# Optimization experiments

Hardware: AMD Instinct MI355X
Metric: run time of the kernel (lower is better)

The kernel has to match this reference:

```python
import jax, jax.numpy as jnp
import numpy as np

N, E = 20000, 320000
IN_DIM, H, C, L = 256, 128, 40, 3
EPS = 1e-5


def _ln(x, g, b):
    mu = jnp.mean(x, axis=-1, keepdims=True)
    var = jnp.mean(jnp.square(x - mu), axis=-1, keepdims=True)
    return (x - mu) * jax.lax.rsqrt(var + EPS) * g + b


def setup_inputs() -> dict:
    key = jax.random.key(0)
    ks = jax.random.split(key, 24)
    s = lambda *sh: 1.0 / np.sqrt(sh[-2] if len(sh) > 1 else sh[-1])
    inp = {
        "x": jax.random.normal(ks[0], (N, IN_DIM), jnp.float32),
        "edge_index": jax.random.randint(ks[1], (2, E), 0, N, jnp.int32),
        "proj_W": jax.random.normal(ks[2], (IN_DIM, H), jnp.float32) / np.sqrt(IN_DIM),
        "proj_b": jnp.zeros((H,), jnp.float32),
        "ln0_g": jnp.ones((H,), jnp.float32),
        "ln0_b": jnp.zeros((H,), jnp.float32),
        "sim_W1": jax.random.normal(ks[3], (L, 3 * H, H), jnp.float32) / np.sqrt(3 * H),
        "sim_b1": jnp.zeros((L, H), jnp.float32),
        "sim_W2": jax.random.normal(ks[4], (L, H, 1), jnp.float32) / np.sqrt(H),
        "sim_b2": jnp.zeros((L, 1), jnp.float32),
        "W_msg": jax.random.normal(ks[5], (L, H, H), jnp.float32) / np.sqrt(H),
        "W_upd": jax.random.normal(ks[6], (L, 2 * H, H), jnp.float32) / np.sqrt(2 * H),
        "b_upd": jnp.zeros((L, H), jnp.float32),
        "ln_g": jnp.ones((L, H), jnp.float32),
        "ln_b": jnp.zeros((L, H), jnp.float32),
        "cls_W1": jax.random.normal(ks[7], (H, H // 2), jnp.float32) / np.sqrt(H),
        "cls_b1": jnp.zeros((H // 2,), jnp.float32),
        "cls_W2": jax.random.normal(ks[8], (H // 2, C), jnp.float32) / np.sqrt(H // 2),
        "cls_b2": jnp.zeros((C,), jnp.float32),
    }
    return inp


def reference(x, edge_index, proj_W, proj_b, ln0_g, ln0_b, sim_W1, sim_b1,
              sim_W2, sim_b2, W_msg, W_upd, b_upd, ln_g, ln_b,
              cls_W1, cls_b1, cls_W2, cls_b2):
    n = x.shape[0]
    # add self loops
    loops = jnp.arange(n, dtype=edge_index.dtype)
    src = jnp.concatenate([edge_index[0], loops])
    dst = jnp.concatenate([edge_index[1], loops])

    h = jax.nn.relu(_ln(x @ proj_W + proj_b, ln0_g, ln0_b))  # (N,H); dropout=eval no-op

    for l in range(L):
        x_i = h[dst]                      # (E',H)
        x_j = h[src]                      # (E',H)
        sim_in = jnp.concatenate([x_i, x_j, jnp.abs(x_i - x_j)], axis=-1)  # (E',3H)
        hmid = jax.nn.relu(sim_in @ sim_W1[l] + sim_b1[l])
        score = jax.nn.sigmoid(hmid @ sim_W2[l] + sim_b2[l])  # (E',1)
        msg = x_j @ W_msg[l]              # (E',H)
        agg = jax.ops.segment_sum(score * msg, dst, num_segments=n)  # (N,H)
        upd = jnp.concatenate([h, agg], axis=-1) @ W_upd[l] + b_upd[l]
        upd = upd + h                     # residual (identity since in==out)
        h = jax.nn.relu(_ln(upd, ln_g[l], ln_b[l]))

    logits = jax.nn.relu(h @ cls_W1 + cls_b1) @ cls_W2 + cls_b2
    return logits
```

## Files before the change

### kernel.cpp

```cpp
#include <hip/hip_runtime.h>
#include <hip/hip_bf16.h>

#define HD 128
#define LN_EPS 1e-5f

typedef __attribute__((ext_vector_type(8))) short short8;
typedef __attribute__((ext_vector_type(4))) float f32x4;

__device__ __forceinline__ unsigned short f2bf(float f) {
    union { float f; unsigned u; } v; v.f = f;
    unsigned r = (v.u + 0x7fffu + ((v.u >> 16) & 1u)) >> 16;
    return (unsigned short)r;
}

__device__ __forceinline__ unsigned cvtpk(float lo, float hi) {
    unsigned r;
    asm("v_cvt_pk_bf16_f32 %0, %1, %2" : "=v"(r) : "v"(lo), "v"(hi));
    return r;
}
__device__ __forceinline__ unsigned cvtpk_abs(float lo, float hi) {
    unsigned r;
    asm("v_cvt_pk_bf16_f32 %0, abs(%1), abs(%2)" : "=v"(r) : "v"(lo), "v"(hi));
    return r;
}
__device__ __forceinline__ unsigned absd_bf2(unsigned a, unsigned b) {
    float alo = __uint_as_float(a << 16), ahi = __uint_as_float(a & 0xffff0000u);
    float blo = __uint_as_float(b << 16), bhi = __uint_as_float(b & 0xffff0000u);
    return cvtpk_abs(alo - blo, ahi - bhi);
}

__device__ __forceinline__ float wave_sum_all(float v) {
    #pragma unroll
    for (int o = 32; o > 0; o >>= 1) v += __shfl_xor(v, o);
    return v;
}

__global__ __launch_bounds__(256) void w1bf_kernel(
    const float* __restrict__ W1, unsigned short* __restrict__ out, int total)
{
    int idx = blockIdx.x * 256 + threadIdx.x;
    if (idx >= total) return;
    int lw  = idx / 49152;
    int rem = idx - lw * 49152;
    int j  = rem & 7;
    int c  = (rem >> 3) & 15;
    int ks = (rem >> 7) & 3;
    int ct = (rem >> 9) & 7;
    int q  = rem >> 12;
    out[idx] = f2bf(W1[(size_t)lw * 49152 + (size_t)(q * 32 + ks * 8 + j) * 128 + ct * 16 + c]);
}

__global__ __launch_bounds__(256) void copy_upd_kernel(
    const float* __restrict__ W_upd, float* __restrict__ wcomb, int total)
{
    int idx = blockIdx.x * 256 + threadIdx.x;
    if (idx >= total) return;
    int l = idx / 16384, r = idx - l * 16384;
    wcomb[(size_t)l * 32768 + r] = W_upd[(size_t)l * 32768 + r];
}

__global__ __launch_bounds__(256) void gemm_rows_kernel(
    const float* __restrict__ in0, int s0, const float* __restrict__ in1, int s1,
    const float* __restrict__ W, const float* __restrict__ bias,
    const float* __restrict__ res, const float* __restrict__ g,
    const float* __restrict__ bln, float* __restrict__ out,
    unsigned* __restrict__ out_bf, int N)
{
    __shared__ __align__(16) float rows[4][8][256];
    int tid = threadIdx.x, wv = tid >> 6, lane = tid & 63;
    int rbase = (blockIdx.x * 4 + wv) * 8;
    if (rbase >= N) return;
    int K = in1 ? 256 : 128;
    int r = lane >> 3, seg = lane & 7;
    int row = min(rbase + r, N - 1);
    {
        const float4* p = (const float4*)(in0 + (size_t)row * s0 + seg * 16);
        float4* q = (float4*)&rows[wv][r][seg * 16];
        #pragma unroll
        for (int i = 0; i < 4; i++) q[i] = p[i];
        if (in1) {
            const float4* p1 = (const float4*)(in1 + (size_t)row * s1 + seg * 16);
            float4* q1 = (float4*)&rows[wv][r][128 + seg * 16];
            #pragma unroll
            for (int i = 0; i < 4; i++) q1[i] = p1[i];
        }
    }
    asm volatile("s_waitcnt lgkmcnt(0)" ::: "memory");
    float2 acc[8];
    float2 bv = make_float2(0.f, 0.f);
    if (bias) bv = *(const float2*)(bias + 2 * lane);
    #pragma unroll
    for (int t = 0; t < 8; t++) acc[t] = bv;
    for (int k = 0; k < K; k += 4) {
        float2 w0 = *(const float2*)(W + (size_t)(k + 0) * 128 + 2 * lane);
        float2 w1 = *(const float2*)(W + (size_t)(k + 1) * 128 + 2 * lane);
        float2 w2 = *(const float2*)(W + (size_t)(k + 2) * 128 + 2 * lane);
        float2 w3 = *(const float2*)(W + (size_t)(k + 3) * 128 + 2 * lane);
        #pragma unroll
        for (int t = 0; t < 8; t++) {
            float4 a = *(const float4*)&rows[wv][t][k];
            acc[t].x = fmaf(a.x, w0.x, acc[t].x); acc[t].y = fmaf(a.x, w0.y, acc[t].y);
            acc[t].x = fmaf(a.y, w1.x, acc[t].x); acc[t].y = fmaf(a.y, w1.y, acc[t].y);
            acc[t].x = fmaf(a.z, w2.x, acc[t].x); acc[t].y = fmaf(a.z, w2.y, acc[t].y);
            acc[t].x = fmaf(a.w, w3.x, acc[t].x); acc[t].y = fmaf(a.w, w3.y, acc[t].y);
        }
    }
    if (res) {
        #pragma unroll
        for (int t = 0; t < 8; t++) {
            int rw = rbase + t;
            if (rw < N) {
                float2 rv = *(const float2*)(res + (size_t)rw * 128 + 2 * lane);
                acc[t].x += rv.x; acc[t].y += rv.y;
            }
        }
    }
    if (g) {
        float2 gv = *(const float2*)(g + 2 * lane);
        float2 lv = *(const float2*)(bln + 2 * lane);
        #pragma unroll
        for (int t = 0; t < 8; t++) {
            int rw = rbase + t;
            if (rw >= N) break;
            float s  = wave_sum_all(acc[t].x + acc[t].y);
            float s2 = wave_sum_all(acc[t].x * acc[t].x + acc[t].y * acc[t].y);
            float mu = s * (1.f / 128.f);
            float var = s2 * (1.f / 128.f) - mu * mu;
            float rs = rsqrtf(var + LN_EPS);
            float2 y;
            y.x = fmaxf((acc[t].x - mu) * rs * gv.x + lv.x, 0.f);
            y.y = fmaxf((acc[t].y - mu) * rs * gv.y + lv.y, 0.f);
            *(float2*)(out + (size_t)rw * 128 + 2 * lane) = y;
            if (out_bf) out_bf[(size_t)rw * 64 + lane] = cvtpk(y.x, y.y);
        }
    } else {
        #pragma unroll
        for (int t = 0; t < 8; t++) {
            int rw = rbase + t;
            if (rw < N) *(float2*)(out + (size_t)rw * 128 + 2 * lane) = acc[t];
        }
    }
}

__global__ __launch_bounds__(256) void hist_kernel(
    const int* __restrict__ dstA, int* __restrict__ cnt, int E, int Etot)
{
    for (int e = blockIdx.x * 256 + threadIdx.x; e < Etot; e += gridDim.x * 256) {
        int di = (e < E) ? dstA[e] : (e - E);
        atomicAdd(&cnt[di], 1);
    }
}

__global__ __launch_bounds__(256) void scan_kernel(
    const int* __restrict__ cnt, int* __restrict__ rowptr, int* __restrict__ cursor,
    int N, int Etot)
{
    __shared__ int ls[256];
    int t = threadIdx.x;
    int chunk = (N + 255) / 256;
    int lo = t * chunk, hi = min(lo + chunk, N);
    int s = 0;
    for (int i = lo; i < hi; i++) s += cnt[i];
    ls[t] = s;
    __syncthreads();
    for (int off = 1; off < 256; off <<= 1) {
        int v = (t >= off) ? ls[t - off] : 0;
        __syncthreads();
        ls[t] += v;
        __syncthreads();
    }
    int run = ls[t] - s;
    for (int i = lo; i < hi; i++) {
        rowptr[i] = run; cursor[i] = run;
        run += cnt[i];
    }
    if (t == 0) rowptr[N] = Etot;
}

__global__ __launch_bounds__(256) void scatter_kernel(
    const int* __restrict__ srcA, const int* __restrict__ dstA,
    int* __restrict__ cursor, int* __restrict__ esrc, int* __restrict__ edst,
    int E, int Etot)
{
    for (int e = blockIdx.x * 256 + threadIdx.x; e < Etot; e += gridDim.x * 256) {
        int si = (e < E) ? srcA[e] : (e - E);
        int di = (e < E) ? dstA[e] : (e - E);
        int pos = atomicAdd(&cursor[di], 1);
        esrc[pos] = si;
        edst[pos] = di;
    }
}

__global__ __launch_bounds__(256, 3) void edge_mfma_kernel(
    const unsigned* __restrict__ hbf,
    const int* __restrict__ esrc, const int* __restrict__ edst,
    const unsigned short* __restrict__ w1bf, const float* __restrict__ b1,
    const float* __restrict__ W2, const float* __restrict__ b2p,
    float* __restrict__ score, int Etot)
{
    __shared__ __align__(16) short sim[3][64][128];
    __shared__ float pl[4][64];
    int tid = threadIdx.x, wv = tid >> 6, lane = tid & 63;
    char* simb = (char*)sim;

    short8 wf[12][2];
    {
        int ks = lane >> 4, c = lane & 15;
        #pragma unroll
        for (int q = 0; q < 12; q++)
            #pragma unroll
            for (int n = 0; n < 2; n++) {
                int ct = wv * 2 + n;
                wf[q][n] = *(const short8*)(w1bf + (size_t)(((q * 8 + ct) * 4 + ks) * 128 + c * 8));
            }
    }
    float b1x = b1[wv * 32 + (lane & 15)],  b1y = b1[wv * 32 + 16 + (lane & 15)];
    float w2x = W2[wv * 32 + (lane & 15)],  w2y = W2[wv * 32 + 16 + (lane & 15)];
    float b2 = b2p[0];

    int nb = gridDim.x;
    int swz = (blockIdx.x & 7) * (nb >> 3) + (blockIdx.x >> 3);
    int ntiles = (Etot + 63) >> 6;
    int t0 = (int)(((long long)ntiles * swz) / nb);
    int t1 = (int)(((long long)ntiles * (swz + 1)) / nb);
    if (t0 >= t1) return;

    int el = tid >> 2, seg = tid & 3;
    int e_cur = min((t0 << 6) + el, Etot - 1);
    int si = esrc[e_cur];
    int di = edst[e_cur];

    for (int tile = t0; tile < t1; tile++) {
        const uint4* xi = (const uint4*)(hbf + (size_t)di * 64 + seg * 16);
        const uint4* xj = (const uint4*)(hbf + (size_t)si * 64 + seg * 16);
        uint4 a0 = xi[0], b0 = xj[0];
        uint4 a1 = xi[1], b1v = xj[1];
        uint4 a2 = xi[2], b2v = xj[2];
        uint4 a3 = xi[3], b3v = xj[3];
        {
            int nt = (tile + 1 < t1) ? (tile + 1) : tile;
            int en = min((nt << 6) + el, Etot - 1);
            si = esrc[en];
            di = edst[en];
        }
        {
            int rowoff = el * 256, sw = (el & 7) << 4;
            uint4 d0, d1, d2, d3;
            d0.x = absd_bf2(a0.x, b0.x); d0.y = absd_bf2(a0.y, b0.y);
            d0.z = absd_bf2(a0.z, b0.z); d0.w = absd_bf2(a0.w, b0.w);
            d1.x = absd_bf2(a1.x, b1v.x); d1.y = absd_bf2(a1.y, b1v.y);
            d1.z = absd_bf2(a1.z, b1v.z); d1.w = absd_bf2(a1.w, b1v.w);
            d2.x = absd_bf2(a2.x, b2v.x); d2.y = absd_bf2(a2.y, b2v.y);
            d2.z = absd_bf2(a2.z, b2v.z); d2.w = absd_bf2(a2.w, b2v.w);
            d3.x = absd_bf2(a3.x, b3v.x); d3.y = absd_bf2(a3.y, b3v.y);
            d3.z = absd_bf2(a3.z, b3v.z); d3.w = absd_bf2(a3.w, b3v.w);
            int o0 = rowoff + ((seg * 64 +  0) ^ sw);
            int o1 = rowoff + ((seg * 64 + 16) ^ sw);
            int o2 = rowoff + ((seg * 64 + 32) ^ sw);
            int o3 = rowoff + ((seg * 64 + 48) ^ sw);
            *(uint4*)(simb + o0)         = a0;  *(uint4*)(simb + o1)         = a1;
            *(uint4*)(simb + o2)         = a2;  *(uint4*)(simb + o3)         = a3;
            *(uint4*)(simb + 16384 + o0) = b0;  *(uint4*)(simb + 16384 + o1) = b1v;
            *(uint4*)(simb + 16384 + o2) = b2v; *(uint4*)(simb + 16384 + o3) = b3v;
            *(uint4*)(simb + 32768 + o0) = d0;  *(uint4*)(simb + 32768 + o1) = d1;
            *(uint4*)(simb + 32768 + o2) = d2;  *(uint4*)(simb + 32768 + o3) = d3;
        }
        __syncthreads();
        f32x4 acc[4][2];
        #pragma unroll
        for (int m = 0; m < 4; m++)
            #pragma unroll
            for (int n = 0; n < 2; n++)
                #pragma unroll
                for (int r = 0; r < 4; r++) acc[m][n][r] = 0.f;
        __builtin_amdgcn_s_setprio(1);
        #pragma unroll
        for (int q = 0; q < 12; q++) {
            int third = q >> 2;
            int kin = ((q & 3) * 64 + (lane >> 4) * 16);
            short8 af[4];
            #pragma unroll
            for (int m = 0; m < 4; m++) {
                int elr = m * 16 + (lane & 15);
                int addr = third * 16384 + elr * 256 + (kin ^ ((elr & 7) << 4));
                af[m] = *(const short8*)(simb + addr);
            }
            #pragma unroll
            for (int m = 0; m < 4; m++)
                #pragma unroll
                for (int n = 0; n < 2; n++)
                    acc[m][n] = __builtin_amdgcn_mfma_f32_16x16x32_bf16(af[m], wf[q][n], acc[m][n], 0, 0, 0);
        }
        __builtin_amdgcn_s_setprio(0);
        int ebase = tile << 6;
        #pragma unroll
        for (int m = 0; m < 4; m++) {
            #pragma unroll
            for (int r = 0; r < 4; r++) {
                float v = fmaxf(acc[m][0][r] + b1x, 0.f) * w2x
                        + fmaxf(acc[m][1][r] + b1y, 0.f) * w2y;
                v += __shfl_xor(v, 1); v += __shfl_xor(v, 2);
                v += __shfl_xor(v, 4); v += __shfl_xor(v, 8);
                if ((lane & 15) == 0) pl[wv][m * 16 + (lane >> 4) * 4 + r] = v;
            }
        }
        __syncthreads();
        if (tid < 64) {
            int e = ebase + tid;
            if (e < Etot) {
                float z = pl[0][tid] + pl[1][tid] + pl[2][tid] + pl[3][tid] + b2;
                score[e] = 1.f / (1.f + __expf(-z));
            }
        }
    }
}

__global__ __launch_bounds__(256) void gather_kernel(
    const int* __restrict__ rowptr, const int* __restrict__ esrc,
    const float* __restrict__ score, const unsigned* __restrict__ hbf,
    float* __restrict__ pre_agg, int N)
{
    int nb = gridDim.x;
    int bid = blockIdx.x;
    int swz = (bid & 7) * (nb >> 3) + (bid >> 3);
    int wvi = threadIdx.x >> 6, lane = threadIdx.x & 63;
    int node = swz * 4 + wvi;
    if (node >= N) return;
    int p0 = rowptr[node], p1 = rowptr[node + 1];
    float2 a0 = make_float2(0.f, 0.f), a1 = a0, a2 = a0, a3 = a0;
    for (int base = p0; base < p1; base += 64) {
        int cnt = min(64, p1 - base);
        int sidx = 0; float sc = 0.f;
        if (lane < cnt) {
            sidx = esrc[base + lane];
            sc = score[base + lane];
        }
        int i = 0;
        for (; i + 4 <= cnt; i += 4) {
            float s0 = __shfl(sc, i),     s1 = __shfl(sc, i + 1);
            float s2 = __shfl(sc, i + 2), s3 = __shfl(sc, i + 3);
            int r0 = __shfl(sidx, i),     r1 = __shfl(sidx, i + 1);
            int r2 = __shfl(sidx, i + 2), r3 = __shfl(sidx, i + 3);
            unsigned u0 = hbf[(size_t)r0 * 64 + lane];
            unsigned u1 = hbf[(size_t)r1 * 64 + lane];
            unsigned u2 = hbf[(size_t)r2 * 64 + lane];
            unsigned u3 = hbf[(size_t)r3 * 64 + lane];
            a0.x = fmaf(s0, __uint_as_float(u0 << 16), a0.x);
            a0.y = fmaf(s0, __uint_as_float(u0 & 0xffff0000u), a0.y);
            a1.x = fmaf(s1, __uint_as_float(u1 << 16), a1.x);
            a1.y = fmaf(s1, __uint_as_float(u1 & 0xffff0000u), a1.y);
            a2.x = fmaf(s2, __uint_as_float(u2 << 16), a2.x);
            a2.y = fmaf(s2, __uint_as_float(u2 & 0xffff0000u), a2.y);
            a3.x = fmaf(s3, __uint_as_float(u3 << 16), a3.x);
            a3.y = fmaf(s3, __uint_as_float(u3 & 0xffff0000u), a3.y);
        }
        for (; i < cnt; i++) {
            float s = __shfl(sc, i);
            int rr = __shfl(sidx, i);
            unsigned u = hbf[(size_t)rr * 64 + lane];
            a0.x = fmaf(s, __uint_as_float(u << 16), a0.x);
            a0.y = fmaf(s, __uint_as_float(u & 0xffff0000u), a0.y);
        }
    }
    float2 o;
    o.x = (a0.x + a1.x) + (a2.x + a3.x);
    o.y = (a0.y + a1.y) + (a2.y + a3.y);
    *(float2*)(pre_agg + (size_t)node * 128 + 2 * lane) = o;
}

__global__ __launch_bounds__(256) void cls_kernel(
    const float* __restrict__ hin, const float* __restrict__ W1,
    const float* __restrict__ b1, const float* __restrict__ W2,
    const float* __restrict__ b2, float* __restrict__ out, int N)
{
    __shared__ __align__(16) float w1[HD * 64];
    __shared__ __align__(16) float w2[64 * 40];
    __shared__ __align__(16) float hs[4][HD];
    __shared__ float ts[4][64];
    for (int i = threadIdx.x; i < HD * 64; i += 256) w1[i] = W1[i];
    for (int i = threadIdx.x; i < 64 * 40; i += 256) w2[i] = W2[i];
    int sub = threadIdx.x >> 6, t = threadIdx.x & 63;
    float b1j = b1[t];
    float b2j = (t < 40) ? b2[t] : 0.f;
    __syncthreads();
    for (int base = blockIdx.x * 4; base < N; base += gridDim.x * 4) {
        int i = base + sub; bool val = i < N;
        if (val) { hs[sub][t] = hin[(size_t)i * HD + t]; hs[sub][64 + t] = hin[(size_t)i * HD + 64 + t]; }
        __syncthreads();
        float acc = b1j;
        const float* hr = hs[sub];
        #pragma unroll 8
        for (int k = 0; k < HD; k += 4) {
            float4 hv = *(const float4*)(hr + k);
            acc = fmaf(hv.x, w1[(k + 0) * 64 + t], acc);
            acc = fmaf(hv.y, w1[(k + 1) * 64 + t], acc);
            acc = fmaf(hv.z, w1[(k + 2) * 64 + t], acc);
            acc = fmaf(hv.w, w1[(k + 3) * 64 + t], acc);
        }
        ts[sub][t] = fmaxf(acc, 0.f);
        __syncthreads();
        if (val && t < 40) {
            float o = b2j;
            const float* tr = ts[sub];
            #pragma unroll 8
            for (int k = 0; k < 64; k++) o = fmaf(tr[k], w2[k * 40 + t], o);
            out[(size_t)i * 40 + t] = o;
        }
        __syncthreads();
    }
}

extern "C" void kernel_launch(void* const* d_in, const int* in_sizes, int n_in,
                              void* d_out, int out_size, void* d_ws, size_t ws_size,
                              hipStream_t stream)
{
    const float* x      = (const float*)d_in[0];
    const int*   ei     = (const int*)d_in[1];
    const float* proj_W = (const float*)d_in[2];
    const float* proj_b = (const float*)d_in[3];
    const float* ln0_g  = (const float*)d_in[4];
    const float* ln0_b  = (const float*)d_in[5];
    const float* sim_W1 = (const float*)d_in[6];
    const float* sim_b1 = (const float*)d_in[7];
    const float* sim_W2 = (const float*)d_in[8];
    const float* sim_b2 = (const float*)d_in[9];
    const float* W_msg  = (const float*)d_in[10];
    const float* W_upd  = (const float*)d_in[11];
    const float* b_upd  = (const float*)d_in[12];
    const float* ln_g   = (const float*)d_in[13];
    const float* ln_b   = (const float*)d_in[14];
    const float* cls_W1 = (const float*)d_in[15];
    const float* cls_b1 = (const float*)d_in[16];
    const float* cls_W2 = (const float*)d_in[17];
    const float* cls_b2 = (const float*)d_in[18];

    int N = in_sizes[0] / 256;
    int E = in_sizes[1] / 2;
    int L = in_sizes[6] / (3 * HD * HD);
    int Etot = E + N;
    const int* srcA = ei;
    const int* dstA = ei + E;

    float* ws = (float*)d_ws;
    size_t nh = (size_t)N * HD;
    float* h       = ws;
    float* pre_agg = h + nh;
    float* score   = pre_agg + nh;
    float* wcomb   = score + Etot + 64;
    unsigned* hbf  = (unsigned*)(wcomb + (size_t)L * 32768);
    unsigned short* w1bf = (unsigned short*)(hbf + nh / 2);
    int*   cnt    = (int*)(w1bf + (size_t)L * 49152);
    int*   rowptr = cnt + N;
    int*   cursor = rowptr + N + 1;
    int*   esrc   = cursor + N;
    int*   edst   = esrc + Etot;

    int gemm_blocks = (N + 31) / 32;

    hipMemsetAsync(cnt, 0, (size_t)N * sizeof(int), stream);
    hist_kernel<<<512, 256, 0, stream>>>(dstA, cnt, E, Etot);
    scan_kernel<<<1, 256, 0, stream>>>(cnt, rowptr, cursor, N, Etot);
    scatter_kernel<<<512, 256, 0, stream>>>(srcA, dstA, cursor, esrc, edst, E, Etot);

    int w1_total = L * 49152;
    w1bf_kernel<<<(w1_total + 255) / 256, 256, 0, stream>>>(sim_W1, w1bf, w1_total);

    int cp_total = L * 16384;
    copy_upd_kernel<<<(cp_total + 255) / 256, 256, 0, stream>>>(W_upd, wcomb, cp_total);
    for (int l = 0; l < L; l++) {
        gemm_rows_kernel<<<(128 + 31) / 32, 256, 0, stream>>>(
            W_msg + (size_t)l * 16384, 128, nullptr, 0,
            W_upd + (size_t)l * 32768 + 16384, nullptr, nullptr, nullptr, nullptr,
            wcomb + (size_t)l * 32768 + 16384, nullptr, 128);
    }

    gemm_rows_kernel<<<gemm_blocks, 256, 0, stream>>>(x, 256, x + 128, 256, proj_W, proj_b,
                                                      nullptr, ln0_g, ln0_b, h, hbf, N);

    int gather_blocks = (N + 3) / 4;
    for (int l = 0; l < L; l++) {
        edge_mfma_kernel<<<768, 256, 0, stream>>>(hbf, esrc, edst,
                                                  w1bf + (size_t)l * 49152, sim_b1 + l * HD,
                                                  sim_W2 + l * HD, sim_b2 + l, score, Etot);
        gather_kernel<<<gather_blocks, 256, 0, stream>>>(rowptr, esrc, score, hbf, pre_agg, N);
        gemm_rows_kernel<<<gemm_blocks, 256, 0, stream>>>(h, 128, pre_agg, 128,
                                                          wcomb + (size_t)l * 32768,
                                                          b_upd + l * HD, h,
                                                          ln_g + l * HD, ln_b + l * HD, h, hbf, N);
    }
    cls_kernel<<<768, 256, 0, stream>>>(h, cls_W1, cls_b1, cls_W2, cls_b2, (float*)d_out, N);
}
```

Measured before the change: 488.4 us.

## Run node update GEMM with bf16 MFMA and store aggregated messages as bf16

Replaces the fp32 row GEMM for the per-layer node update with a new bf16 MFMA kernel. That kernel reads h and the aggregate in bf16, fuses bias, residual, LayerNorm and ReLU, and writes both fp32 h and bf16 h. The gather kernel now packs its output to bf16, which halves the aggregate traffic, and the combined update weights are pre-converted into an MFMA fragment layout. This lowers precision on the update inputs and computes variance as E[x^2]-mu^2, so accuracy may drift slightly.

```diff
diff --git a/kernel.cpp b/kernel.cpp
--- a/kernel.cpp
+++ b/kernel.cpp
@@ -48,6 +48,21 @@
     int ct = (rem >> 9) & 7;
     int q  = rem >> 12;
     out[idx] = f2bf(W1[(size_t)lw * 49152 + (size_t)(q * 32 + ks * 8 + j) * 128 + ct * 16 + c]);
+}
+
+__global__ __launch_bounds__(256) void wcbf_kernel(
+    const float* __restrict__ wcomb, unsigned short* __restrict__ out, int total)
+{
+    int idx = blockIdx.x * 256 + threadIdx.x;
+    if (idx >= total) return;
+    int lw  = idx >> 15;
+    int rem = idx & 32767;
+    int j  = rem & 7;
+    int c  = (rem >> 3) & 15;
+    int ks = (rem >> 7) & 3;
+    int ct = (rem >> 9) & 7;
+    int q  = rem >> 12;
+    out[idx] = f2bf(wcomb[(size_t)lw * 32768 + (size_t)(q * 32 + ks * 8 + j) * 128 + ct * 16 + c]);
 }
 
 __global__ __launch_bounds__(256) void copy_upd_kernel(
@@ -246,8 +261,8 @@
         {
             int rowoff = el * 256, sw = (el & 7) << 4;
             uint4 d0, d1, d2, d3;
-            d0.x = absd_bf2(a0.x, b0.x); d0.y = absd_bf2(a0.y, b0.y);
-            d0.z = absd_bf2(a0.z, b0.z); d0.w = absd_bf2(a0.w, b0.w);
+            d0.x = absd_bf2(a0.x, b0.x);  d0.y = absd_bf2(a0.y, b0.y);
+            d0.z = absd_bf2(a0.z, b0.z);  d0.w = absd_bf2(a0.w, b0.w);
             d1.x = absd_bf2(a1.x, b1v.x); d1.y = absd_bf2(a1.y, b1v.y);
             d1.z = absd_bf2(a1.z, b1v.z); d1.w = absd_bf2(a1.w, b1v.w);
             d2.x = absd_bf2(a2.x, b2v.x); d2.y = absd_bf2(a2.y, b2v.y);
@@ -318,7 +333,7 @@
 __global__ __launch_bounds__(256) void gather_kernel(
     const int* __restrict__ rowptr, const int* __restrict__ esrc,
     const float* __restrict__ score, const unsigned* __restrict__ hbf,
-    float* __restrict__ pre_agg, int N)
+    unsigned* __restrict__ paggbf, int N)
 {
     int nb = gridDim.x;
     int bid = blockIdx.x;
@@ -362,10 +377,105 @@
             a0.y = fmaf(s, __uint_as_float(u & 0xffff0000u), a0.y);
         }
     }
-    float2 o;
-    o.x = (a0.x + a1.x) + (a2.x + a3.x);
-    o.y = (a0.y + a1.y) + (a2.y + a3.y);
-    *(float2*)(pre_agg + (size_t)node * 128 + 2 * lane) = o;
+    float ox = (a0.x + a1.x) + (a2.x + a3.x);
+    float oy = (a0.y + a1.y) + (a2.y + a3.y);
+    paggbf[(size_t)node * 64 + lane] = cvtpk(ox, oy);
+}
+
+__global__ __launch_bounds__(256, 3) void upd_mfma_kernel(
+    const unsigned* __restrict__ hbf, const unsigned* __restrict__ paggbf,
+    const float* __restrict__ hres,
+    const unsigned short* __restrict__ wcbf,
+    const float* __restrict__ bias, const float* __restrict__ g,
+    const float* __restrict__ bln,
+    float* __restrict__ hout, unsigned* __restrict__ hbf_out, int N)
+{
+    __shared__ float ps[4][64], pq[4][64];
+    int tid = threadIdx.x, wv = tid >> 6, lane = tid & 63;
+    int c = lane & 15, l16 = lane >> 4;
+    int rbase = blockIdx.x * 64;
+    if (rbase >= N) return;
+
+    short8 wf[8][2];
+    #pragma unroll
+    for (int q = 0; q < 8; q++)
+        #pragma unroll
+        for (int n = 0; n < 2; n++) {
+            int ct = wv * 2 + n;
+            wf[q][n] = *(const short8*)(wcbf + (size_t)(((q * 8 + ct) * 4 + l16) * 128 + c * 8));
+        }
+    float g0  = g[wv * 32 + c],    g1  = g[wv * 32 + 16 + c];
+    float lb0 = bln[wv * 32 + c],  lb1 = bln[wv * 32 + 16 + c];
+    float bs0 = bias[wv * 32 + c], bs1 = bias[wv * 32 + 16 + c];
+
+    f32x4 acc[4][2];
+    #pragma unroll
+    for (int m = 0; m < 4; m++)
+        #pragma unroll
+        for (int n = 0; n < 2; n++)
+            #pragma unroll
+            for (int r = 0; r < 4; r++) acc[m][n][r] = 0.f;
+
+    int arow[4];
+    #pragma unroll
+    for (int m = 0; m < 4; m++) arow[m] = min(rbase + m * 16 + c, N - 1);
+
+    #pragma unroll
+    for (int q = 0; q < 8; q++) {
+        const unsigned* src = (q < 4) ? hbf : paggbf;
+        int qq = (q < 4) ? q : q - 4;
+        short8 af[4];
+        #pragma unroll
+        for (int m = 0; m < 4; m++)
+            af[m] = *(const short8*)(src + (size_t)arow[m] * 64 + qq * 16 + l16 * 4);
+        #pragma unroll
+        for (int m = 0; m < 4; m++)
+            #pragma unroll
+            for (int n = 0; n < 2; n++)
+                acc[m][n] = __builtin_amdgcn_mfma_f32_16x16x32_bf16(af[m], wf[q][n], acc[m][n], 0, 0, 0);
+    }
+
+    #pragma unroll
+    for (int m = 0; m < 4; m++) {
+        #pragma unroll
+        for (int r = 0; r < 4; r++) {
+            int rit = m * 16 + l16 * 4 + r;
+            int rowc = min(rbase + rit, N - 1);
+            float v0 = acc[m][0][r] + bs0 + hres[(size_t)rowc * 128 + wv * 32 + c];
+            float v1 = acc[m][1][r] + bs1 + hres[(size_t)rowc * 128 + wv * 32 + 16 + c];
+            acc[m][0][r] = v0; acc[m][1][r] = v1;
+            float s = v0 + v1, sq = v0 * v0 + v1 * v1;
+            s  += __shfl_xor(s, 1);  s  += __shfl_xor(s, 2);  s  += __shfl_xor(s, 4);  s  += __shfl_xor(s, 8);
+            sq += __shfl_xor(sq, 1); sq += __shfl_xor(sq, 2); sq += __shfl_xor(sq, 4); sq += __shfl_xor(sq, 8);
+            if (c == 0) { ps[wv][rit] = s; pq[wv][rit] = sq; }
+        }
+    }
+    __syncthreads();
+    #pragma unroll
+    for (int m = 0; m < 4; m++) {
+        #pragma unroll
+        for (int r = 0; r < 4; r++) {
+            int rit = m * 16 + l16 * 4 + r;
+            int row = rbase + rit;
+            float s  = (ps[0][rit] + ps[1][rit]) + (ps[2][rit] + ps[3][rit]);
+            float sq = (pq[0][rit] + pq[1][rit]) + (pq[2][rit] + pq[3][rit]);
+            float mu = s * (1.f / 128.f);
+            float var = sq * (1.f / 128.f) - mu * mu;
+            float rs = rsqrtf(var + LN_EPS);
+            float y0 = fmaxf((acc[m][0][r] - mu) * rs * g0 + lb0, 0.f);
+            float y1 = fmaxf((acc[m][1][r] - mu) * rs * g1 + lb1, 0.f);
+            float z0 = __shfl_xor(y0, 1);
+            float z1 = __shfl_xor(y1, 1);
+            if (row < N) {
+                hout[(size_t)row * 128 + wv * 32 + c]      = y0;
+                hout[(size_t)row * 128 + wv * 32 + 16 + c] = y1;
+                if (!(lane & 1)) {
+                    hbf_out[(size_t)row * 64 + wv * 16 + (c >> 1)]     = cvtpk(y0, z0);
+                    hbf_out[(size_t)row * 64 + wv * 16 + 8 + (c >> 1)] = cvtpk(y1, z1);
+                }
+            }
+        }
+    }
 }
 
 __global__ __launch_bounds__(256) void cls_kernel(
@@ -443,13 +553,14 @@
 
     float* ws = (float*)d_ws;
     size_t nh = (size_t)N * HD;
-    float* h       = ws;
-    float* pre_agg = h + nh;
-    float* score   = pre_agg + nh;
-    float* wcomb   = score + Etot + 64;
-    unsigned* hbf  = (unsigned*)(wcomb + (size_t)L * 32768);
-    unsigned short* w1bf = (unsigned short*)(hbf + nh / 2);
-    int*   cnt    = (int*)(w1bf + (size_t)L * 49152);
+    float* h      = ws;
+    float* score  = h + nh;
+    float* wcomb  = score + Etot + 64;
+    unsigned* hbf    = (unsigned*)(wcomb + (size_t)L * 32768);
+    unsigned* paggbf = hbf + nh / 2;
+    unsigned short* w1bf = (unsigned short*)(paggbf + nh / 2);
+    unsigned short* wcbf = w1bf + (size_t)L * 49152;
+    int*   cnt    = (int*)(wcbf + (size_t)L * 32768);
     int*   rowptr = cnt + N;
     int*   cursor = rowptr + N + 1;
     int*   esrc   = cursor + N;
@@ -473,20 +584,23 @@
             W_upd + (size_t)l * 32768 + 16384, nullptr, nullptr, nullptr, nullptr,
             wcomb + (size_t)l * 32768 + 16384, nullptr, 128);
     }
+    int wc_total = L * 32768;
+    wcbf_kernel<<<(wc_total + 255) / 256, 256, 0, stream>>>(wcomb, wcbf, wc_total);
 
     gemm_rows_kernel<<<gemm_blocks, 256, 0, stream>>>(x, 256, x + 128, 256, proj_W, proj_b,
                                                       nullptr, ln0_g, ln0_b, h, hbf, N);
 
     int gather_blocks = (N + 3) / 4;
+    int upd_blocks = (N + 63) / 64;
     for (int l = 0; l < L; l++) {
         edge_mfma_kernel<<<768, 256, 0, stream>>>(hbf, esrc, edst,
                                                   w1bf + (size_t)l * 49152, sim_b1 + l * HD,
                                                   sim_W2 + l * HD, sim_b2 + l, score, Etot);
-        gather_kernel<<<gather_blocks, 256, 0, stream>>>(rowptr, esrc, score, hbf, pre_agg, N);
-        gemm_rows_kernel<<<gemm_blocks, 256, 0, stream>>>(h, 128, pre_agg, 128,
-                                                          wcomb + (size_t)l * 32768,
-                                                          b_upd + l * HD, h,
-                                                          ln_g + l * HD, ln_b + l * HD, h, hbf, N);
+        gather_kernel<<<gather_blocks, 256, 0, stream>>>(rowptr, esrc, score, hbf, paggbf, N);
+        upd_mfma_kernel<<<upd_blocks, 256, 0, stream>>>(hbf, paggbf, h,
+                                                        wcbf + (size_t)l * 32768,
+                                                        b_upd + l * HD, ln_g + l * HD, ln_b + l * HD,
+                                                        h, hbf, N);
     }
     cls_kernel<<<768, 256, 0, stream>>>(h, cls_W1, cls_b1, cls_W2, cls_b2, (float*)d_out, N);
 }
```

Result: faster. 454.7 us (-6.9%).
